# Optimization experiments

Hardware: AMD Instinct MI355X
Metric: run time of the kernel (lower is better)

Reference implementation:

```python
import jax, jax.numpy as jnp
import numpy as np

TOP_K = 15
TEMPERATURE = 1.0
NEG_SLOPE = 0.2


def setup_inputs() -> dict:
    key = jax.random.key(0)
    ks = jax.random.split(key, 6)
    N, H, heads, hd = 4096, 256, 4, 64
    E_c = 131072
    embeddings = jax.random.normal(ks[0], (N, H), dtype=jnp.float32)
    # nn.Linear(H, heads*hd, bias=False) weight: [heads*hd, H], xavier-ish scale
    W = jax.random.normal(ks[1], (heads * hd, H), dtype=jnp.float32) * (1.0 / np.sqrt(H))
    att = jax.random.normal(ks[2], (heads, 2 * hd), dtype=jnp.float32) * 0.1
    corr_lambda = jnp.ones((1,), dtype=jnp.float32)
    sector_mask = jax.random.uniform(ks[3], (N, N)) > 0.05
    active_mask = jnp.ones((N,), dtype=bool)
    corr_edge_index = jax.random.randint(ks[4], (2, E_c), 0, N)
    corr_edge_weight = jax.random.uniform(ks[5], (E_c,), minval=-1.0, maxval=1.0)
    return dict(embeddings=embeddings, W=W, att=att, corr_lambda=corr_lambda,
                sector_mask=sector_mask, active_mask=active_mask,
                corr_edge_index=corr_edge_index, corr_edge_weight=corr_edge_weight)


def reference(embeddings, W, att, corr_lambda, sector_mask, active_mask,
              corr_edge_index, corr_edge_weight):
    N = embeddings.shape[0]
    heads = att.shape[0]
    hd = att.shape[1] // 2
    # h: [N, heads, hd]
    h = (embeddings @ W.T).reshape(N, heads, hd)
    # algebraic split of concat([h_i || h_j]) . att  ->  s_dst[i] + s_src[j]
    a_dst, a_src = att[:, :hd], att[:, hd:]
    s_dst = jnp.einsum('nhd,hd->nh', h, a_dst)  # coefficient of row node i
    s_src = jnp.einsum('nhd,hd->nh', h, a_src)  # coefficient of col node j
    # [N, N, heads] broadcast-add, leaky_relu, mean over heads
    scores = jax.nn.leaky_relu(s_dst[:, None, :] + s_src[None, :, :], NEG_SLOPE)
    scores = scores.mean(axis=-1) / TEMPERATURE  # [N, N]
    mask = (active_mask[:, None] & active_mask[None, :]) & sector_mask  # [N, N]
    scores = jnp.where(mask, scores, -jnp.inf)
    # correlation prior scattered into a dense matrix (index-assign semantics)
    corr = jnp.zeros((N, N), dtype=scores.dtype).at[
        corr_edge_index[0], corr_edge_index[1]].set(corr_edge_weight.astype(scores.dtype))
    corr = corr * mask.astype(scores.dtype)
    scores = scores + corr_lambda[0] * corr
    k = min(TOP_K, N - 1)
    topk_scores, topk_idx = jax.lax.top_k(scores, k)  # per-row top-k over src dim
    rows = jnp.broadcast_to(jnp.arange(N)[:, None], (N, k))
    # dense mask guarantees all top-k entries are finite -> E = N*k fixed
    edge_index = jnp.stack([topk_idx.reshape(-1), rows.reshape(-1)], axis=0)  # [2, N*k]
    edge_weight = jax.nn.softmax(topk_scores, axis=1).reshape(-1)  # [N*k]
    return edge_index, edge_weight
```

## Files before the change

kernel.cpp:

```cpp
#include <hip/hip_runtime.h>
#include <math.h>

#define H_DIM 256
#define HEADS 4
#define HD 64
#define TOPK 15
#define NSLOPE 0.2
#define NSLOPEF 0.2f
#define EDGE_CAP_MAX 128
#define CAND_CAP 256
#define SROWS 16

__global__ __launch_bounds__(256) void prep1_kernel(const float* __restrict__ W,
                                                    const float* __restrict__ att,
                                                    double* __restrict__ wa_dst,
                                                    double* __restrict__ wa_src,
                                                    int* __restrict__ cnt,
                                                    unsigned int* __restrict__ abits,
                                                    const int* __restrict__ active) {
    const int b = blockIdx.x;
    cnt[b * 256 + threadIdx.x] = 0;
    if (b < 2 * HEADS) {
        const int k = threadIdx.x;
        const int h = b >> 1;
        const int side = b & 1;
        double a = 0.0;
        for (int d = 0; d < HD; ++d)
            a += (double)W[(h * HD + d) * H_DIM + k] * (double)att[h * 2 * HD + side * HD + d];
        (side ? wa_src : wa_dst)[h * H_DIM + k] = a;
    } else if (b == 8 && threadIdx.x < 128) {
        const int* ap = active + threadIdx.x * 32;
        unsigned int wv = 0;
        for (int t = 0; t < 32; ++t)
            if (ap[t]) wv |= 1u << t;
        abits[threadIdx.x] = wv;
    }
}

__global__ __launch_bounds__(256) void prep2_kernel(
    const float* __restrict__ emb, const double* __restrict__ wa_dst,
    const double* __restrict__ wa_src, double* __restrict__ s_dst,
    double* __restrict__ s_src, float* __restrict__ s_dst_f,
    float* __restrict__ s_src_f, const int* __restrict__ eidx,
    const float* __restrict__ ew, int* __restrict__ cnt,
    int4* __restrict__ etab, int N, int E, int cap, int sblocks) {
    const int b = blockIdx.x;
    const int tid = threadIdx.x;

    if (b < sblocks) {
        __shared__ double wa_l[8][258];
        __shared__ float emb_l[SROWS][258];
        const int i0 = b * SROWS;
#pragma unroll
        for (int c = 0; c < 8; ++c)
            wa_l[c][tid] = ((c & 1) ? wa_src : wa_dst)[(c >> 1) * H_DIM + tid];
#pragma unroll
        for (int r = 0; r < SROWS; ++r)
            emb_l[r][tid] = emb[(size_t)(i0 + r) * H_DIM + tid];
        __syncthreads();

        const int j = tid >> 1;
        const int half = tid & 1;
        const int r = j >> 3;
        const int c = j & 7;
        const int base = half * 128;
        double acc = 0.0;
#pragma unroll 8
        for (int k = 0; k < 128; ++k)
            acc += (double)emb_l[r][base + k] * wa_l[c][base + k];
        const double other = __shfl_xor(acc, 1, 64);
        const double lo = half ? other : acc;
        const double hi = half ? acc : other;
        const double s = lo + hi;
        if (half == 0) {
            const int i = i0 + r;
            const int h = c >> 1;
            if (c & 1) {
                s_src[i * HEADS + h] = s;
                s_src_f[i * HEADS + h] = (float)s;
            } else {
                s_dst[i * HEADS + h] = s;
                s_dst_f[i * HEADS + h] = (float)s;
            }
        }
    } else {
        const int e = (b - sblocks) * 256 + tid;
        if (e < E) {
            const int r = eidx[e];
            const int cc = eidx[E + e];
            const int s = atomicAdd(&cnt[r], 1);
            if (s < cap) {
                int4 rec;
                rec.x = cc;
                rec.y = e;
                rec.z = __float_as_int(ew[e]);
                rec.w = 0;
                etab[r * cap + s] = rec;
            }
        }
    }
}

#define FOR16(OP) OP(0) OP(1) OP(2) OP(3) OP(4) OP(5) OP(6) OP(7) \
                  OP(8) OP(9) OP(10) OP(11) OP(12) OP(13) OP(14) OP(15)

__global__ __launch_bounds__(256, 8) void main_kernel(
    const double* __restrict__ s_dst, const double* __restrict__ s_src,
    const float* __restrict__ s_dst_f, const float* __restrict__ s_src_f,
    const int* __restrict__ sector_mask, const unsigned short* __restrict__ abits16,
    const int* __restrict__ active, const float* __restrict__ lam_p,
    const int* __restrict__ cnt, const int4* __restrict__ etab,
    float* __restrict__ out, int N, int cap) {
    const int i = blockIdx.x;
    const int tid = threadIdx.x;
    const int lane = tid & 63;
    const int wid = tid >> 6;

    __shared__ int ec[EDGE_CAP_MAX];
    __shared__ int ee[EDGE_CAP_MAX];
    __shared__ float ewl[EDGE_CAP_MAX];
    __shared__ double wadd[EDGE_CAP_MAX];
    __shared__ unsigned short tab16[4096];
    __shared__ float waddf[EDGE_CAP_MAX + 2];
    __shared__ unsigned int wth[4];
    __shared__ double cand_v[CAND_CAP];
    __shared__ int cand_i[CAND_CAP];
    __shared__ int cand_cnt, wcnt;
    __shared__ double sorted_v[TOPK];
    __shared__ int sorted_i[TOPK];
    __shared__ double exps[TOPK];

    const int* mrow = sector_mask + (size_t)i * N;
    const int4 m0 = *(const int4*)(mrow + 16 * tid);
    const int4 m1 = *(const int4*)(mrow + 16 * tid + 4);
    const int4 m2 = *(const int4*)(mrow + 16 * tid + 8);
    const int4 m3 = *(const int4*)(mrow + 16 * tid + 12);
    const unsigned int act_us = (unsigned int)abits16[tid];

    if (tid == 0) { cand_cnt = 0; wcnt = 0; waddf[0] = 0.0f; }

    {
        int* t4 = (int*)tab16;
#pragma unroll
        for (int z = 0; z < 8; ++z) t4[tid + (z << 8)] = 0;
    }

    int deg = cnt[i];
    if (deg > cap) deg = cap;
    for (int p = tid; p < deg; p += 256) {
        const int4 rec = etab[i * cap + p];
        ec[p] = rec.x;
        ee[p] = rec.y;
        ewl[p] = __int_as_float(rec.z);
    }

    unsigned int pb = 0;
#define PB(C, VAL) if ((VAL) != 0) pb |= (1u << (C));
    PB(0, m0.x)  PB(1, m0.y)  PB(2, m0.z)  PB(3, m0.w)
    PB(4, m1.x)  PB(5, m1.y)  PB(6, m1.z)  PB(7, m1.w)
    PB(8, m2.x)  PB(9, m2.y)  PB(10, m2.z) PB(11, m2.w)
    PB(12, m3.x) PB(13, m3.y) PB(14, m3.z) PB(15, m3.w)
#undef PB
    pb &= act_us;

    const int lhi = lane >> 4;
    const int llo = lane & 15;
    unsigned int pm = 0;
#pragma unroll
    for (int k = 0; k < 16; ++k) {
        const unsigned int opb = (unsigned int)__shfl((int)pb, 4 * k + lhi, 64);
        pm |= ((opb >> llo) & 1u) << k;
    }
    if (active[i] == 0) pm = 0;

    __syncthreads();

    const float sdf0 = s_dst_f[i * 4 + 0];
    const float sdf1 = s_dst_f[i * 4 + 1];
    const float sdf2 = s_dst_f[i * 4 + 2];
    const float sdf3 = s_dst_f[i * 4 + 3];
    const double sd0 = s_dst[i * 4 + 0];
    const double sd1 = s_dst[i * 4 + 1];
    const double sd2 = s_dst[i * 4 + 2];
    const double sd3 = s_dst[i * 4 + 3];
    const double lam = (double)lam_p[0];
    const double4* __restrict__ s_src4 = (const double4*)s_src;
    const float4* __restrict__ s_srcf4 = (const float4*)s_src_f;
    const int jbase = (wid << 10) | lane;

    float f0, f1, f2, f3, f4, f5, f6, f7, f8, f9, f10, f11, f12, f13, f14, f15;
#define INIT_SLOT(K) { \
    const bool m = (pm >> K) & 1u; \
    const float4 sv = s_srcf4[jbase + (K << 6)]; \
    float x0 = sdf0 + sv.x, x1 = sdf1 + sv.y, x2 = sdf2 + sv.z, x3 = sdf3 + sv.w; \
    x0 = (x0 < 0.0f) ? NSLOPEF * x0 : x0; \
    x1 = (x1 < 0.0f) ? NSLOPEF * x1 : x1; \
    x2 = (x2 < 0.0f) ? NSLOPEF * x2 : x2; \
    x3 = (x3 < 0.0f) ? NSLOPEF * x3 : x3; \
    f##K = m ? (0.25f * (x0 + x1 + x2 + x3)) : -INFINITY; }
    FOR16(INIT_SLOT)
#undef INIT_SLOT

    if (tid < deg) {
        const int c = ec[tid];
        const int eid = ee[tid];
        bool win = true;
        for (int q = 0; q < deg; ++q)
            if (ec[q] == c && ee[q] > eid) win = false;
        if (win) {
            const double a = lam * (double)ewl[tid];
            int p = atomicAdd(&wcnt, 1);
            wadd[p] = a;
            waddf[p + 1] = (float)a;
            tab16[c] = (unsigned short)(p + 1);
        }
    }
    __syncthreads();

#define ADDG(K) f##K += waddf[tab16[jbase + (K << 6)]];
    FOR16(ADDG)
#undef ADDG

    unsigned int k0, k1, k2, k3, k4, k5, k6, k7, k8, k9, k10, k11, k12, k13, k14, k15;
#define KEY_SLOT(K) { const unsigned u = __float_as_uint(f##K); \
    k##K = u ^ ((unsigned)((int)u >> 31) | 0x80000000u); }
    FOR16(KEY_SLOT)
#undef KEY_SLOT
    unsigned int lmax = k0;
#define LMAX(K) if (k##K > lmax) lmax = k##K;
    FOR16(LMAX)
#undef LMAX

    unsigned int th = 0;
    for (int b = 31; b >= 8; --b) {
        const unsigned int trial = th | (1u << b);
        unsigned long long m = __ballot(lmax >= trial);
        if (__popcll(m) >= TOPK) th = trial;
    }
    if (lane == 0) wth[wid] = th;
    __syncthreads();
    th = wth[0];
    if (wth[1] > th) th = wth[1];
    if (wth[2] > th) th = wth[2];
    if (wth[3] > th) th = wth[3];
    th = (th > 256u) ? (th - 256u) : 0u;

#define FILT(K) if (k##K >= th) { int p = atomicAdd(&cand_cnt, 1); \
    if (p < CAND_CAP) cand_i[p] = jbase + (K << 6); }
    FOR16(FILT)
#undef FILT
    __syncthreads();

    int C = cand_cnt;
    if (C > CAND_CAP) C = CAND_CAP;
    if (tid < C) {
        const int j = cand_i[tid];
        const double4 sv = s_src4[j];
        double x0 = sd0 + sv.x, x1 = sd1 + sv.y, x2 = sd2 + sv.z, x3 = sd3 + sv.w;
        x0 = (x0 < 0.0) ? NSLOPE * x0 : x0;
        x1 = (x1 < 0.0) ? NSLOPE * x1 : x1;
        x2 = (x2 < 0.0) ? NSLOPE * x2 : x2;
        x3 = (x3 < 0.0) ? NSLOPE * x3 : x3;
        double v = 0.25 * (x0 + x1 + x2 + x3);
        const int slot = tab16[j];
        if (slot) v += wadd[slot - 1];
        cand_v[tid] = v;
    }
    __syncthreads();

    if (tid < C) {
        const double mv = cand_v[tid];
        const int mi = cand_i[tid];
        int rank = 0;
        for (int q = 0; q < C; ++q) {
            const double qv = cand_v[q];
            const int qi = cand_i[q];
            rank += ((qv > mv) || (qv == mv && qi < mi)) ? 1 : 0;
        }
        if (rank < TOPK) { sorted_v[rank] = mv; sorted_i[rank] = mi; }
    }
    __syncthreads();

    if (tid < TOPK) exps[tid] = exp(sorted_v[tid] - sorted_v[0]);
    __syncthreads();
    if (tid < TOPK) {
        double s = 0.0;
        for (int t = 0; t < TOPK; ++t) s += exps[t];
        const int NK = N * TOPK;
        const int base = i * TOPK + tid;
        out[base] = (float)sorted_i[tid];
        out[NK + base] = (float)i;
        out[2 * NK + base] = (float)(exps[tid] / s);
    }
}

extern "C" void kernel_launch(void* const* d_in, const int* in_sizes, int n_in,
                              void* d_out, int out_size, void* d_ws, size_t ws_size,
                              hipStream_t stream) {
    const float* emb    = (const float*)d_in[0];
    const float* W      = (const float*)d_in[1];
    const float* att    = (const float*)d_in[2];
    const float* lam    = (const float*)d_in[3];
    const int*   sector = (const int*)d_in[4];
    const int*   active = (const int*)d_in[5];
    const int*   eidx   = (const int*)d_in[6];
    const float* ew     = (const float*)d_in[7];
    float* out = (float*)d_out;

    const int N = in_sizes[5];
    const int E = in_sizes[6] / 2;

    double* wa_dst = (double*)d_ws;
    double* wa_src = wa_dst + HEADS * H_DIM;
    double* s_dst  = wa_src + HEADS * H_DIM;
    double* s_src  = s_dst + (size_t)N * HEADS;
    float* s_dst_f = (float*)(s_src + (size_t)N * HEADS);
    float* s_src_f = s_dst_f + (size_t)N * HEADS;
    int* cnt       = (int*)(s_src_f + (size_t)N * HEADS);
    unsigned int* abits = (unsigned int*)(cnt + N);
    uintptr_t ep = (uintptr_t)(abits + N / 32);
    ep = (ep + 15) & ~(uintptr_t)15;
    int4* etab = (int4*)ep;

    size_t used = (ep - (uintptr_t)d_ws) + 64;
    size_t rem = (ws_size > used) ? (ws_size - used) : 0;
    int cap = (int)(rem / ((size_t)N * 16));
    if (cap > EDGE_CAP_MAX) cap = EDGE_CAP_MAX;
    if (cap < 16) cap = 16;

    const int nb = (E + 255) / 256;
    const int sblocks = N / SROWS;

    prep1_kernel<<<16, 256, 0, stream>>>(W, att, wa_dst, wa_src, cnt, abits, active);
    prep2_kernel<<<sblocks + nb, 256, 0, stream>>>(emb, wa_dst, wa_src, s_dst, s_src,
                                                   s_dst_f, s_src_f, eidx, ew, cnt,
                                                   etab, N, E, cap, sblocks);
    main_kernel<<<N, 256, 0, stream>>>(s_dst, s_src, s_dst_f, s_src_f, sector,
                                       (const unsigned short*)abits, active, lam, cnt,
                                       etab, out, N, cap);
}
```

Measured before the change: 157.4 us.

## Move sector-mask bit packing from main kernel into prep2 kernel

The sector mask read and bit packing move out of the main kernel into extra blocks of the prep2 kernel. Those blocks write a compact 16-bit-per-thread packed mask to workspace, and the main kernel reads that instead of the full int mask row. The 64 MB mask stream now runs alongside the projection and edge-table blocks, leaving the main kernel lighter. In exchange there is an extra 2 MB write and read round trip, a larger workspace, and a smaller edge-table cap if workspace is tight.

Result: slower. 161.6 us (+2.7%).

```diff
diff --git a/kernel.cpp b/kernel.cpp
--- a/kernel.cpp
+++ b/kernel.cpp
@@ -43,14 +43,42 @@
     double* __restrict__ s_src, float* __restrict__ s_dst_f,
     float* __restrict__ s_src_f, const int* __restrict__ eidx,
     const float* __restrict__ ew, int* __restrict__ cnt,
-    int4* __restrict__ etab, int N, int E, int cap, int sblocks) {
+    int4* __restrict__ etab, const int* __restrict__ sector_mask,
+    const unsigned short* __restrict__ abits16, const int* __restrict__ active,
+    unsigned short* __restrict__ packed, int N, int E, int cap, int sblocks) {
     const int b = blockIdx.x;
     const int tid = threadIdx.x;
 
-    if (b < sblocks) {
+    if (b < N) {
+        const int i = b;
+        const int lane = tid & 63;
+        const int* mrow = sector_mask + (size_t)i * N;
+        const int4 m0 = *(const int4*)(mrow + 16 * tid);
+        const int4 m1 = *(const int4*)(mrow + 16 * tid + 4);
+        const int4 m2 = *(const int4*)(mrow + 16 * tid + 8);
+        const int4 m3 = *(const int4*)(mrow + 16 * tid + 12);
+        unsigned int pb = 0;
+#define PB(C, VAL) if ((VAL) != 0) pb |= (1u << (C));
+        PB(0, m0.x)  PB(1, m0.y)  PB(2, m0.z)  PB(3, m0.w)
+        PB(4, m1.x)  PB(5, m1.y)  PB(6, m1.z)  PB(7, m1.w)
+        PB(8, m2.x)  PB(9, m2.y)  PB(10, m2.z) PB(11, m2.w)
+        PB(12, m3.x) PB(13, m3.y) PB(14, m3.z) PB(15, m3.w)
+#undef PB
+        pb &= (unsigned int)abits16[tid];
+        const int lhi = lane >> 4;
+        const int llo = lane & 15;
+        unsigned int pm = 0;
+#pragma unroll
+        for (int k = 0; k < 16; ++k) {
+            const unsigned int opb = (unsigned int)__shfl((int)pb, 4 * k + lhi, 64);
+            pm |= ((opb >> llo) & 1u) << k;
+        }
+        if (active[i] == 0) pm = 0;
+        packed[i * 256 + tid] = (unsigned short)pm;
+    } else if (b < N + sblocks) {
         __shared__ double wa_l[8][258];
         __shared__ float emb_l[SROWS][258];
-        const int i0 = b * SROWS;
+        const int i0 = (b - N) * SROWS;
 #pragma unroll
         for (int c = 0; c < 8; ++c)
             wa_l[c][tid] = ((c & 1) ? wa_src : wa_dst)[(c >> 1) * H_DIM + tid];
@@ -84,7 +112,7 @@
             }
         }
     } else {
-        const int e = (b - sblocks) * 256 + tid;
+        const int e = (b - N - sblocks) * 256 + tid;
         if (e < E) {
             const int r = eidx[e];
             const int cc = eidx[E + e];
@@ -107,8 +135,7 @@
 __global__ __launch_bounds__(256, 8) void main_kernel(
     const double* __restrict__ s_dst, const double* __restrict__ s_src,
     const float* __restrict__ s_dst_f, const float* __restrict__ s_src_f,
-    const int* __restrict__ sector_mask, const unsigned short* __restrict__ abits16,
-    const int* __restrict__ active, const float* __restrict__ lam_p,
+    const unsigned short* __restrict__ packed, const float* __restrict__ lam_p,
     const int* __restrict__ cnt, const int4* __restrict__ etab,
     float* __restrict__ out, int N, int cap) {
     const int i = blockIdx.x;
@@ -130,12 +157,7 @@
     __shared__ int sorted_i[TOPK];
     __shared__ double exps[TOPK];
 
-    const int* mrow = sector_mask + (size_t)i * N;
-    const int4 m0 = *(const int4*)(mrow + 16 * tid);
-    const int4 m1 = *(const int4*)(mrow + 16 * tid + 4);
-    const int4 m2 = *(const int4*)(mrow + 16 * tid + 8);
-    const int4 m3 = *(const int4*)(mrow + 16 * tid + 12);
-    const unsigned int act_us = (unsigned int)abits16[tid];
+    const unsigned int pm = (unsigned int)packed[i * 256 + tid];
 
     if (tid == 0) { cand_cnt = 0; wcnt = 0; waddf[0] = 0.0f; }
 
@@ -153,26 +175,6 @@
         ee[p] = rec.y;
         ewl[p] = __int_as_float(rec.z);
     }
-
-    unsigned int pb = 0;
-#define PB(C, VAL) if ((VAL) != 0) pb |= (1u << (C));
-    PB(0, m0.x)  PB(1, m0.y)  PB(2, m0.z)  PB(3, m0.w)
-    PB(4, m1.x)  PB(5, m1.y)  PB(6, m1.z)  PB(7, m1.w)
-    PB(8, m2.x)  PB(9, m2.y)  PB(10, m2.z) PB(11, m2.w)
-    PB(12, m3.x) PB(13, m3.y) PB(14, m3.z) PB(15, m3.w)
-#undef PB
-    pb &= act_us;
-
-    const int lhi = lane >> 4;
-    const int llo = lane & 15;
-    unsigned int pm = 0;
-#pragma unroll
-    for (int k = 0; k < 16; ++k) {
-        const unsigned int opb = (unsigned int)__shfl((int)pb, 4 * k + lhi, 64);
-        pm |= ((opb >> llo) & 1u) << k;
-    }
-    if (active[i] == 0) pm = 0;
-
     __syncthreads();
 
     const float sdf0 = s_dst_f[i * 4 + 0];
@@ -318,7 +320,8 @@
     float* s_src_f = s_dst_f + (size_t)N * HEADS;
     int* cnt       = (int*)(s_src_f + (size_t)N * HEADS);
     unsigned int* abits = (unsigned int*)(cnt + N);
-    uintptr_t ep = (uintptr_t)(abits + N / 32);
+    unsigned short* packed = (unsigned short*)(abits + N / 32);
+    uintptr_t ep = (uintptr_t)(packed + (size_t)N * 256);
     ep = (ep + 15) & ~(uintptr_t)15;
     int4* etab = (int4*)ep;
 
@@ -332,10 +335,12 @@
     const int sblocks = N / SROWS;
 
     prep1_kernel<<<16, 256, 0, stream>>>(W, att, wa_dst, wa_src, cnt, abits, active);
-    prep2_kernel<<<sblocks + nb, 256, 0, stream>>>(emb, wa_dst, wa_src, s_dst, s_src,
-                                                   s_dst_f, s_src_f, eidx, ew, cnt,
-                                                   etab, N, E, cap, sblocks);
-    main_kernel<<<N, 256, 0, stream>>>(s_dst, s_src, s_dst_f, s_src_f, sector,
-                                       (const unsigned short*)abits, active, lam, cnt,
-                                       etab, out, N, cap);
+    prep2_kernel<<<N + sblocks + nb, 256, 0, stream>>>(emb, wa_dst, wa_src, s_dst,
+                                                       s_src, s_dst_f, s_src_f, eidx,
+                                                       ew, cnt, etab, sector,
+                                                       (const unsigned short*)abits,
+                                                       active, packed, N, E, cap,
+                                                       sblocks);
+    main_kernel<<<N, 256, 0, stream>>>(s_dst, s_src, s_dst_f, s_src_f, packed, lam,
+                                       cnt, etab, out, N, cap);
 }
```
